# Kernel tuning notes

Hardware: AMD Instinct MI355X
Metric: run time of the kernel (lower is better)

The kernel has to match this reference:

```python
import jax, jax.numpy as jnp
import numpy as np

B, C, O, H, W = 4, 64, 64, 96, 320


def _conv(x, w, b):
    # NCHW conv, stride 1, SAME padding (matches pad=kernel//2 in the torch code)
    out = jax.lax.conv_general_dilated(x, w, (1, 1), 'SAME',
                                       dimension_numbers=('NCHW', 'OIHW', 'NCHW'))
    return out + b[None, :, None, None]


def setup_inputs() -> dict:
    key = jax.random.key(0)
    ks = jax.random.split(key, 18)
    s = 0.05  # small init so learned offsets stay in a realistic few-pixel range
    d = {}
    d['x'] = jax.random.normal(ks[0], (B, C, H, W), jnp.float32)
    d['scale_box2d'] = jax.random.uniform(ks[1], (B, 5), jnp.float32, 0.0, 100.0)
    d['glob_w1'] = jax.random.normal(ks[2], (64, 2), jnp.float32) * s
    d['glob_b1'] = jnp.zeros((64,), jnp.float32)
    d['glob_w2'] = jax.random.normal(ks[3], (32, 64), jnp.float32) * s
    d['glob_b2'] = jnp.zeros((32,), jnp.float32)
    d['loc_w1'] = jax.random.normal(ks[4], (32, C, 3, 3), jnp.float32) * s
    d['loc_b1'] = jnp.zeros((32,), jnp.float32)
    d['loc_w2'] = jax.random.normal(ks[5], (32, 32, 1, 1), jnp.float32) * s
    d['loc_b2'] = jnp.zeros((32,), jnp.float32)
    d['fuse_w1'] = jax.random.normal(ks[6], (32, 64, 3, 3), jnp.float32) * s
    d['fuse_b1'] = jnp.zeros((32,), jnp.float32)
    d['fuse_w2'] = jax.random.normal(ks[7], (18, 32, 1, 1), jnp.float32) * s
    d['fuse_b2'] = jnp.zeros((18,), jnp.float32)
    d['mask_w'] = jnp.full((9, C, 3, 3), 0.5, jnp.float32)  # matches init_mask in torch code
    d['mask_b'] = jnp.zeros((9,), jnp.float32)
    d['conv_w'] = jax.random.normal(ks[8], (O, C, 3, 3), jnp.float32) * s
    d['conv_b'] = jax.random.normal(ks[9], (O,), jnp.float32) * s
    return d


def _deform_conv2d(x, offset, mask, weight, bias):
    # torchvision.ops.deform_conv2d, 3x3 kernel, stride 1, pad 1, dilation 1,
    # one offset group. offset channels are (dy, dx) interleaved per kernel tap.
    b, c, h, w = x.shape
    K = 9
    off = offset.reshape(b, K, 2, h, w)
    dy, dx = off[:, :, 0], off[:, :, 1]            # [B,K,H,W]
    ki = jnp.arange(3, dtype=jnp.float32) - 1.0     # kernel tap offsets with pad=1
    ky = jnp.repeat(ki, 3)                          # [9] row-major taps
    kx = jnp.tile(ki, 3)
    ys = jnp.arange(h, dtype=jnp.float32)[None, None, :, None] + ky[None, :, None, None] + dy
    xs = jnp.arange(w, dtype=jnp.float32)[None, None, None, :] + kx[None, :, None, None] + dx

    y0 = jnp.floor(ys).astype(jnp.int32)
    x0 = jnp.floor(xs).astype(jnp.int32)
    wy = (ys - y0.astype(jnp.float32))[:, None]     # [B,1,K,H,W]
    wx = (xs - x0.astype(jnp.float32))[:, None]

    xf = x.reshape(b, c, h * w)

    def gather(yi, xi):
        valid = ((yi >= 0) & (yi < h) & (xi >= 0) & (xi < w))
        yc = jnp.clip(yi, 0, h - 1)
        xc = jnp.clip(xi, 0, w - 1)
        idx = (yc * w + xc).reshape(b, 1, K * h * w)
        g = jnp.take_along_axis(xf, idx, axis=2).reshape(b, c, K, h, w)
        return g * valid.astype(x.dtype)[:, None]

    val = (gather(y0, x0) * (1 - wy) * (1 - wx)
           + gather(y0, x0 + 1) * (1 - wy) * wx
           + gather(y0 + 1, x0) * wy * (1 - wx)
           + gather(y0 + 1, x0 + 1) * wy * wx)   # [B,C,K,H,W]

    val = val * mask[:, None]                      # modulation mask [B,1,K,H,W]
    out = jnp.einsum('bckhw,ock->bohw', val, weight.reshape(weight.shape[0], c, K))
    return out + bias[None, :, None, None]


def reference(x, scale_box2d, glob_w1, glob_b1, glob_w2, glob_b2,
              loc_w1, loc_b1, loc_w2, loc_b2,
              fuse_w1, fuse_b1, fuse_w2, fuse_b2,
              mask_w, mask_b, conv_w, conv_b):
    b, c, h, w = x.shape
    bsize = jnp.stack([scale_box2d[:, 4] - scale_box2d[:, 2],
                       scale_box2d[:, 3] - scale_box2d[:, 1]], axis=-1)  # [B,2]
    g = jax.nn.relu(bsize @ glob_w1.T + glob_b1) @ glob_w2.T + glob_b2   # [B,32]
    g_offset = jnp.broadcast_to(g[:, :, None, None], (b, 32, h, w))
    l = _conv(jax.nn.relu(_conv(x, loc_w1, loc_b1)), loc_w2, loc_b2)     # [B,32,H,W]
    f = jax.nn.relu(_conv(jnp.concatenate([g_offset, l], axis=1), fuse_w1, fuse_b1))
    offset = _conv(f, fuse_w2, fuse_b2)                                  # [B,18,H,W]
    mask = jax.nn.sigmoid(_conv(x, mask_w, mask_b))                      # [B,9,H,W]
    return _deform_conv2d(x, offset, mask, conv_w, conv_b)
```

## Files before the change

kernel.cpp:

```cpp
#include <hip/hip_runtime.h>
#include <hip/hip_bf16.h>
#include <math.h>

#define BB 4
#define CC 64
#define OO 64
#define HH 96
#define WW 320
#define HWP (HH*WW)
#define NPIX (BB*HWP)

typedef __attribute__((ext_vector_type(8))) short bf16x8;
typedef __attribute__((ext_vector_type(4))) float f32x4;

__device__ inline unsigned short f2bf(float f) {
    unsigned int u = __float_as_uint(f);
    u = (u + 0x7FFFu + ((u >> 16) & 1u)) >> 16;
    return (unsigned short)u;
}
__device__ inline float bf2f(unsigned short s) {
    return __uint_as_float(((unsigned int)s) << 16);
}

__global__ void k_glob(const float* __restrict__ sb,
                       const float* __restrict__ gw1, const float* __restrict__ gb1,
                       const float* __restrict__ gw2, const float* __restrict__ gb2,
                       const float* __restrict__ fw1,
                       float* __restrict__ gsum) {
    __shared__ float g_s[BB * 32];
    int tid = threadIdx.x;
    if (tid < 128) {
        int b = tid >> 5, i = tid & 31;
        float b0 = sb[b * 5 + 4] - sb[b * 5 + 2];
        float b1 = sb[b * 5 + 3] - sb[b * 5 + 1];
        float acc = gb2[i];
        for (int j = 0; j < 64; ++j) {
            float h1 = b0 * gw1[j * 2 + 0] + b1 * gw1[j * 2 + 1] + gb1[j];
            h1 = fmaxf(h1, 0.f);
            acc += gw2[i * 64 + j] * h1;
        }
        g_s[b * 32 + i] = acc;
    }
    __syncthreads();
    for (int e = tid; e < BB * 32 * 9; e += blockDim.x) {
        int b = e / 288, r = e % 288, o = r / 9, k = r % 9;
        float s = 0.f;
        for (int ci = 0; ci < 32; ++ci)
            s += g_s[b * 32 + ci] * fw1[o * 576 + ci * 9 + k];
        gsum[e] = s;
    }
}

#define PREP_N (36864 + 27648 + 1024 + 9216 + 1024)
__global__ void k_prep(const float* __restrict__ cw,
                       const float* __restrict__ lw1, const float* __restrict__ mw,
                       const float* __restrict__ lw2,
                       const float* __restrict__ fw1, const float* __restrict__ fw2,
                       unsigned short* __restrict__ cwT,
                       unsigned short* __restrict__ Wlm,
                       unsigned short* __restrict__ lw2T,
                       unsigned short* __restrict__ Wf,
                       unsigned short* __restrict__ fw2A) {
    int e = blockIdx.x * 256 + threadIdx.x;
    if (e < 36864) {
        int k = e >> 12, r = e & 4095, o = r >> 6, ci = r & 63;
        cwT[e] = f2bf(cw[o * 576 + ci * 9 + k]);
        return;
    }
    e -= 36864;
    if (e < 27648) {
        int k = e / 3072, r = e % 3072, row = r >> 6, ci = r & 63;
        float v = 0.f;
        if (row < 32) v = lw1[row * 576 + ci * 9 + k];
        else if (row < 41) v = mw[(row - 32) * 576 + ci * 9 + k];
        Wlm[e] = f2bf(v);
        return;
    }
    e -= 27648;
    if (e < 1024) { lw2T[e] = f2bf(lw2[e]); return; }
    e -= 1024;
    if (e < 9216) {
        int k = e >> 10, r = e & 1023, o = r >> 5, cl = r & 31;
        Wf[e] = f2bf(fw1[o * 576 + (32 + cl) * 9 + k]);
        return;
    }
    e -= 9216;
    if (e < 1024) {
        int m = e >> 5, ci = e & 31;
        fw2A[e] = f2bf(m < 18 ? fw2[m * 32 + ci] : 0.f);
    }
}

__global__ __launch_bounds__(256) void k_xT(const float* __restrict__ x,
                                            unsigned short* __restrict__ xT) {
    __shared__ unsigned short Ls[64 * 66];
    int tid = threadIdx.x;
    int p0 = blockIdx.x * 64;
    int b = p0 / HWP;
    int rem0 = p0 % HWP;
    int px = tid & 63;
    int g4 = tid >> 6;
    const float* xb = x + (size_t)b * CC * HWP + rem0;
#pragma unroll
    for (int it = 0; it < 16; ++it) {
        int ci = it * 4 + g4;
        Ls[px * 66 + ci] = f2bf(xb[(size_t)ci * HWP + px]);
    }
    __syncthreads();
#pragma unroll
    for (int it = 0; it < 16; ++it) {
        int p = it * 4 + g4;
        xT[(size_t)(p0 + p) * 64 + px] = Ls[p * 66 + px];
    }
}

__global__ __launch_bounds__(256) void k_locmask(
        const unsigned short* __restrict__ xT,
        const unsigned short* __restrict__ Wlm,
        const unsigned short* __restrict__ lw2T,
        const float* __restrict__ lb1, const float* __restrict__ lb2,
        const float* __restrict__ mb,
        unsigned short* __restrict__ lT, unsigned short* __restrict__ mbuf) {
    __shared__ unsigned short Vs[128 * 72];
    __shared__ unsigned short Ws[48 * 72];
    __shared__ unsigned short VsL[128 * 40];
    __shared__ unsigned short W2[32 * 40];

    int tid = threadIdx.x;
    int p0 = blockIdx.x * 128;
    int rem0 = p0 % HWP;

    int lane = tid & 63, wv = tid >> 6;
    int lr = lane & 15, lq = lane >> 4;
    int n0 = wv * 32;

    int spx = tid >> 1;
    int shf = tid & 1;
    int sy = (rem0 + spx) / WW;
    int sx = (rem0 + spx) % WW;

    f32x4 acc[3][2];
#pragma unroll
    for (int mt = 0; mt < 3; ++mt)
#pragma unroll
        for (int t = 0; t < 2; ++t) acc[mt][t] = (f32x4){0.f, 0.f, 0.f, 0.f};

    for (int k = 0; k < 9; ++k) {
        int dy = k / 3 - 1, dx = k % 3 - 1;
        __syncthreads();
#pragma unroll
        for (int c = tid; c < 384; c += 256) {
            int row = c >> 3, g = c & 7;
            *(float4*)&Ws[row * 72 + g * 8] =
                *(const float4*)&Wlm[((size_t)k * 48 + row) * 64 + g * 8];
        }
        {
            int yy = sy + dy, xw = sx + dx;
            bool valid = (yy >= 0) && (yy < HH) && (xw >= 0) && (xw < WW);
            unsigned short* dst = &Vs[spx * 72 + shf * 32];
            if (valid) {
                const unsigned short* src =
                    xT + ((size_t)(p0 + spx) + (dy * WW + dx)) * 64 + shf * 32;
#pragma unroll
                for (int j = 0; j < 4; ++j)
                    *(float4*)(dst + j * 8) = *(const float4*)(src + j * 8);
            } else {
                float4 z = {0.f, 0.f, 0.f, 0.f};
#pragma unroll
                for (int j = 0; j < 4; ++j) *(float4*)(dst + j * 8) = z;
            }
        }
        __syncthreads();
#pragma unroll
        for (int h = 0; h < 2; ++h) {
            bf16x8 b0 = *(const bf16x8*)&Vs[(n0 + lr) * 72 + h * 32 + lq * 8];
            bf16x8 b1 = *(const bf16x8*)&Vs[(n0 + 16 + lr) * 72 + h * 32 + lq * 8];
#pragma unroll
            for (int mt = 0; mt < 3; ++mt) {
                bf16x8 a = *(const bf16x8*)&Ws[(mt * 16 + lr) * 72 + h * 32 + lq * 8];
                acc[mt][0] = __builtin_amdgcn_mfma_f32_16x16x32_bf16(a, b0, acc[mt][0], 0, 0, 0);
                acc[mt][1] = __builtin_amdgcn_mfma_f32_16x16x32_bf16(a, b1, acc[mt][1], 0, 0, 0);
            }
        }
    }

#pragma unroll
    for (int c = tid; c < 128; c += 256) {
        int row = c >> 2, g = c & 3;
        *(float4*)&W2[row * 40 + g * 8] = *(const float4*)&lw2T[row * 32 + g * 8];
    }
#pragma unroll
    for (int mt = 0; mt < 2; ++mt)
#pragma unroll
        for (int t = 0; t < 2; ++t)
#pragma unroll
            for (int r = 0; r < 4; ++r) {
                int m = mt * 16 + lq * 4 + r;
                float v = acc[mt][t][r] + lb1[m];
                VsL[(n0 + t * 16 + lr) * 40 + m] = f2bf(fmaxf(v, 0.f));
            }
#pragma unroll
    for (int t = 0; t < 2; ++t)
#pragma unroll
        for (int r = 0; r < 4; ++r) {
            int j = lq * 4 + r;
            if (j < 9) {
                float v = acc[2][t][r] + mb[j];
                v = 1.f / (1.f + __expf(-v));
                mbuf[(size_t)j * NPIX + p0 + n0 + t * 16 + lr] = f2bf(v);
            }
        }
    __syncthreads();
    f32x4 acc2[2][2];
#pragma unroll
    for (int mt = 0; mt < 2; ++mt)
#pragma unroll
        for (int t = 0; t < 2; ++t) acc2[mt][t] = (f32x4){0.f, 0.f, 0.f, 0.f};
#pragma unroll
    for (int t = 0; t < 2; ++t) {
        bf16x8 b2 = *(const bf16x8*)&VsL[(n0 + t * 16 + lr) * 40 + lq * 8];
#pragma unroll
        for (int mt = 0; mt < 2; ++mt) {
            bf16x8 a2 = *(const bf16x8*)&W2[(mt * 16 + lr) * 40 + lq * 8];
            acc2[mt][t] = __builtin_amdgcn_mfma_f32_16x16x32_bf16(a2, b2, acc2[mt][t], 0, 0, 0);
        }
    }
    __syncthreads();
#pragma unroll
    for (int mt = 0; mt < 2; ++mt)
#pragma unroll
        for (int t = 0; t < 2; ++t)
#pragma unroll
            for (int r = 0; r < 4; ++r) {
                int m = mt * 16 + lq * 4 + r;
                Vs[(n0 + t * 16 + lr) * 40 + m] = f2bf(acc2[mt][t][r] + lb2[m]);
            }
    __syncthreads();
    {
        int px = tid >> 1, hf = tid & 1;
        float4 v0 = *(const float4*)&Vs[px * 40 + hf * 16];
        float4 v1 = *(const float4*)&Vs[px * 40 + hf * 16 + 8];
        unsigned short* dst = lT + (size_t)(p0 + px) * 32 + hf * 16;
        *(float4*)dst = v0;
        *(float4*)(dst + 8) = v1;
    }
}

__global__ __launch_bounds__(256) void k_fuse(
        const unsigned short* __restrict__ lT,
        const float* __restrict__ gsum,
        const unsigned short* __restrict__ Wf,
        const unsigned short* __restrict__ fw2A,
        const float* __restrict__ fb1, const float* __restrict__ fb2,
        float* __restrict__ ysA, float* __restrict__ xsA) {
    __shared__ unsigned short Vs[128 * 40];
    __shared__ unsigned short Ws[32 * 40];
    __shared__ unsigned short VsF[128 * 40];
    __shared__ unsigned short W2[32 * 40];
    __shared__ float gs[288];

    int tid = threadIdx.x;
    int p0 = blockIdx.x * 128;
    int b = p0 / HWP;
    int rem0 = p0 % HWP;

    int lane = tid & 63, wv = tid >> 6;
    int lr = lane & 15, lq = lane >> 4;
    int n0 = wv * 32;

    int spx = tid >> 1;
    int shf = tid & 1;
    int sy = (rem0 + spx) / WW;
    int sx = (rem0 + spx) % WW;

    for (int e = tid; e < 288; e += 256) gs[e] = gsum[b * 288 + e];

    f32x4 acc[2][2];
#pragma unroll
    for (int mt = 0; mt < 2; ++mt)
#pragma unroll
        for (int t = 0; t < 2; ++t) acc[mt][t] = (f32x4){0.f, 0.f, 0.f, 0.f};

    for (int k = 0; k < 9; ++k) {
        int dy = k / 3 - 1, dx = k % 3 - 1;
        __syncthreads();
#pragma unroll
        for (int c = tid; c < 128; c += 256) {
            int row = c >> 2, g = c & 3;
            *(float4*)&Ws[row * 40 + g * 8] =
                *(const float4*)&Wf[((size_t)k * 32 + row) * 32 + g * 8];
        }
        {
            int yy = sy + dy, xw = sx + dx;
            bool valid = (yy >= 0) && (yy < HH) && (xw >= 0) && (xw < WW);
            unsigned short* dst = &Vs[spx * 40 + shf * 16];
            if (valid) {
                const unsigned short* src =
                    lT + ((size_t)(p0 + spx) + (dy * WW + dx)) * 32 + shf * 16;
                *(float4*)dst = *(const float4*)src;
                *(float4*)(dst + 8) = *(const float4*)(src + 8);
            } else {
                float4 z = {0.f, 0.f, 0.f, 0.f};
                *(float4*)dst = z;
                *(float4*)(dst + 8) = z;
            }
        }
        __syncthreads();
#pragma unroll
        for (int t = 0; t < 2; ++t) {
            bf16x8 bfr = *(const bf16x8*)&Vs[(n0 + t * 16 + lr) * 40 + lq * 8];
#pragma unroll
            for (int mt = 0; mt < 2; ++mt) {
                bf16x8 a = *(const bf16x8*)&Ws[(mt * 16 + lr) * 40 + lq * 8];
                acc[mt][t] = __builtin_amdgcn_mfma_f32_16x16x32_bf16(a, bfr, acc[mt][t], 0, 0, 0);
            }
        }
    }

#pragma unroll
    for (int c = tid; c < 128; c += 256) {
        int row = c >> 2, g = c & 3;
        *(float4*)&W2[row * 40 + g * 8] = *(const float4*)&fw2A[row * 32 + g * 8];
    }
#pragma unroll
    for (int t = 0; t < 2; ++t) {
        int px = n0 + t * 16 + lr;
        int rem = rem0 + px;
        int y = rem / WW, xx = rem % WW;
        bool vk[9];
#pragma unroll
        for (int k = 0; k < 9; ++k) {
            int yy = y + k / 3 - 1, xw = xx + k % 3 - 1;
            vk[k] = (yy >= 0) && (yy < HH) && (xw >= 0) && (xw < WW);
        }
#pragma unroll
        for (int mt = 0; mt < 2; ++mt)
#pragma unroll
            for (int r = 0; r < 4; ++r) {
                int m = mt * 16 + lq * 4 + r;
                float s = fb1[m];
#pragma unroll
                for (int k = 0; k < 9; ++k)
                    if (vk[k]) s += gs[m * 9 + k];
                float v = acc[mt][t][r] + s;
                VsF[px * 40 + m] = f2bf(fmaxf(v, 0.f));
            }
    }
    __syncthreads();
    f32x4 acc3[2][2];
#pragma unroll
    for (int mt = 0; mt < 2; ++mt)
#pragma unroll
        for (int t = 0; t < 2; ++t) acc3[mt][t] = (f32x4){0.f, 0.f, 0.f, 0.f};
#pragma unroll
    for (int t = 0; t < 2; ++t) {
        bf16x8 b2 = *(const bf16x8*)&VsF[(n0 + t * 16 + lr) * 40 + lq * 8];
#pragma unroll
        for (int mt = 0; mt < 2; ++mt) {
            bf16x8 a2 = *(const bf16x8*)&W2[(mt * 16 + lr) * 40 + lq * 8];
            acc3[mt][t] = __builtin_amdgcn_mfma_f32_16x16x32_bf16(a2, b2, acc3[mt][t], 0, 0, 0);
        }
    }
#pragma unroll
    for (int t = 0; t < 2; ++t) {
        int px = n0 + t * 16 + lr;
        int p = p0 + px;
        int rem = rem0 + px;
        int y = rem / WW, xx = rem % WW;
#pragma unroll
        for (int mt = 0; mt < 2; ++mt)
#pragma unroll
            for (int r = 0; r < 4; ++r) {
                int m = mt * 16 + lq * 4 + r;
                if (m < 18) {
                    int k = m >> 1;
                    float v = acc3[mt][t][r] + fb2[m];
                    if ((m & 1) == 0)
                        ysA[(size_t)k * NPIX + p] = (float)(y + k / 3 - 1) + v;
                    else
                        xsA[(size_t)k * NPIX + p] = (float)(xx + k % 3 - 1) + v;
                }
            }
    }
}

__global__ __launch_bounds__(256) void k_deform(
        const unsigned short* __restrict__ xT,
        const unsigned short* __restrict__ cwT, const float* __restrict__ cb,
        const float* __restrict__ ysA, const float* __restrict__ xsA,
        const unsigned short* __restrict__ mA, float* __restrict__ out) {
    __shared__ unsigned short Vs[64 * 72];
    __shared__ unsigned short Ws[64 * 72];
    __shared__ float4 cfA[9 * 64];
    __shared__ int4   igA[9 * 64];

    int tid = threadIdx.x;
    int p0 = blockIdx.x * 64;
    int b = p0 / HWP;
    int rem0 = p0 % HWP;
    const unsigned short* xTb = xT + (size_t)b * HWP * 64;

    for (int e = tid; e < 9 * 64; e += 256) {
        int k = e / 64, px = e % 64;
        int p = p0 + px;
        float ys = ysA[(size_t)k * NPIX + p];
        float xs = xsA[(size_t)k * NPIX + p];
        float mk = bf2f(mA[(size_t)k * NPIX + p]);
        float y0f = floorf(ys), x0f = floorf(xs);
        int y0 = (int)y0f, x0 = (int)x0f;
        float wy = ys - y0f, wx = xs - x0f;
        float c00 = (1.f - wy) * (1.f - wx) * mk;
        float c01 = (1.f - wy) * wx * mk;
        float c10 = wy * (1.f - wx) * mk;
        float c11 = wy * wx * mk;
        bool vy0 = (y0 >= 0) && (y0 < HH);
        bool vy1 = (y0 + 1 >= 0) && (y0 + 1 < HH);
        bool vx0 = (x0 >= 0) && (x0 < WW);
        bool vx1 = (x0 + 1 >= 0) && (x0 + 1 < WW);
        c00 = (vy0 && vx0) ? c00 : 0.f;
        c01 = (vy0 && vx1) ? c01 : 0.f;
        c10 = (vy1 && vx0) ? c10 : 0.f;
        c11 = (vy1 && vx1) ? c11 : 0.f;
        int yc0 = min(max(y0, 0), HH - 1), yc1 = min(max(y0 + 1, 0), HH - 1);
        int xc0 = min(max(x0, 0), WW - 1), xc1 = min(max(x0 + 1, 0), WW - 1);
        cfA[e] = make_float4(c00, c01, c10, c11);
        igA[e] = make_int4((yc0 * WW + xc0) * 64, (yc0 * WW + xc1) * 64,
                           (yc1 * WW + xc0) * 64, (yc1 * WW + xc1) * 64);
    }

    int lane = tid & 63;
    int wv = tid >> 6;
    int m0 = wv * 16;
    int lr = lane & 15;
    int lq = lane >> 4;

    f32x4 cini;
    cini[0] = cb[m0 + lq * 4 + 0];
    cini[1] = cb[m0 + lq * 4 + 1];
    cini[2] = cb[m0 + lq * 4 + 2];
    cini[3] = cb[m0 + lq * 4 + 3];
    f32x4 acc[4];
#pragma unroll
    for (int t = 0; t < 4; ++t) acc[t] = cini;

    int sgc = tid & 15;
    int sci0 = sgc * 4;
    int spx = tid >> 4;

    for (int k = 0; k < 9; ++k) {
        __syncthreads();
#pragma unroll
        for (int c = tid; c < 512; c += 256) {
            int o = c >> 3, g = c & 7;
            *(float4*)&Ws[o * 72 + g * 8] = ((const float4*)(cwT + (size_t)k * 4096))[c];
        }
#pragma unroll
        for (int q = 0; q < 4; ++q) {
            int px = q * 16 + spx;
            float4 cc = cfA[k * 64 + px];
            int4 ii = igA[k * 64 + px];
            ushort4 u00 = *(const ushort4*)&xTb[ii.x + sci0];
            ushort4 u01 = *(const ushort4*)&xTb[ii.y + sci0];
            ushort4 u10 = *(const ushort4*)&xTb[ii.z + sci0];
            ushort4 u11 = *(const ushort4*)&xTb[ii.w + sci0];
            ushort4 r;
            r.x = f2bf(cc.x * bf2f(u00.x) + cc.y * bf2f(u01.x) + cc.z * bf2f(u10.x) + cc.w * bf2f(u11.x));
            r.y = f2bf(cc.x * bf2f(u00.y) + cc.y * bf2f(u01.y) + cc.z * bf2f(u10.y) + cc.w * bf2f(u11.y));
            r.z = f2bf(cc.x * bf2f(u00.z) + cc.y * bf2f(u01.z) + cc.z * bf2f(u10.z) + cc.w * bf2f(u11.z));
            r.w = f2bf(cc.x * bf2f(u00.w) + cc.y * bf2f(u01.w) + cc.z * bf2f(u10.w) + cc.w * bf2f(u11.w));
            *(ushort4*)&Vs[px * 72 + sci0] = r;
        }
        __syncthreads();
        bf16x8 a0 = *(const bf16x8*)&Ws[(m0 + lr) * 72 + lq * 8];
        bf16x8 a1 = *(const bf16x8*)&Ws[(m0 + lr) * 72 + 32 + lq * 8];
#pragma unroll
        for (int t = 0; t < 4; ++t) {
            bf16x8 b0 = *(const bf16x8*)&Vs[(t * 16 + lr) * 72 + lq * 8];
            bf16x8 b1 = *(const bf16x8*)&Vs[(t * 16 + lr) * 72 + 32 + lq * 8];
            acc[t] = __builtin_amdgcn_mfma_f32_16x16x32_bf16(a0, b0, acc[t], 0, 0, 0);
            acc[t] = __builtin_amdgcn_mfma_f32_16x16x32_bf16(a1, b1, acc[t], 0, 0, 0);
        }
    }

#pragma unroll
    for (int t = 0; t < 4; ++t) {
#pragma unroll
        for (int r = 0; r < 4; ++r) {
            int o = m0 + lq * 4 + r;
            out[(size_t)(b * 64 + o) * HWP + rem0 + t * 16 + lr] = acc[t][r];
        }
    }
}

extern "C" void kernel_launch(void* const* d_in, const int* in_sizes, int n_in,
                              void* d_out, int out_size, void* d_ws, size_t ws_size,
                              hipStream_t stream) {
    const float* x   = (const float*)d_in[0];
    const float* sb  = (const float*)d_in[1];
    const float* gw1 = (const float*)d_in[2];
    const float* gb1 = (const float*)d_in[3];
    const float* gw2 = (const float*)d_in[4];
    const float* gb2 = (const float*)d_in[5];
    const float* lw1 = (const float*)d_in[6];
    const float* lb1 = (const float*)d_in[7];
    const float* lw2 = (const float*)d_in[8];
    const float* lb2 = (const float*)d_in[9];
    const float* fw1 = (const float*)d_in[10];
    const float* fb1 = (const float*)d_in[11];
    const float* fw2 = (const float*)d_in[12];
    const float* fb2 = (const float*)d_in[13];
    const float* mw  = (const float*)d_in[14];
    const float* mb  = (const float*)d_in[15];
    const float* cw  = (const float*)d_in[16];
    const float* cb  = (const float*)d_in[17];
    float* out = (float*)d_out;

    char* w = (char*)d_ws;
    float* gsum = (float*)w;                 w += 1152 * 4;
    unsigned short* cwT  = (unsigned short*)w; w += 36864 * 2;
    unsigned short* Wlm  = (unsigned short*)w; w += 27648 * 2;
    unsigned short* lw2T = (unsigned short*)w; w += 1024 * 2;
    unsigned short* Wf   = (unsigned short*)w; w += 9216 * 2;
    unsigned short* fw2A = (unsigned short*)w; w += 1024 * 2;
    unsigned short* mbuf = (unsigned short*)w; w += (size_t)9 * NPIX * 2;
    float* ysA = (float*)w;                  w += (size_t)9 * NPIX * 4;
    float* xsA = (float*)w;                  w += (size_t)9 * NPIX * 4;
    unsigned short* xT = (unsigned short*)w; w += (size_t)NPIX * 64 * 2;
    unsigned short* lT = (unsigned short*)w;

    k_prep<<<(PREP_N + 255) / 256, 256, 0, stream>>>(cw, lw1, mw, lw2, fw1, fw2,
                                                     cwT, Wlm, lw2T, Wf, fw2A);
    k_glob<<<1, 128, 0, stream>>>(sb, gw1, gb1, gw2, gb2, fw1, gsum);
    k_xT<<<NPIX / 64, 256, 0, stream>>>(x, xT);
    k_locmask<<<NPIX / 128, 256, 0, stream>>>(xT, Wlm, lw2T, lb1, lb2, mb, lT, mbuf);
    k_fuse<<<NPIX / 128, 256, 0, stream>>>(lT, gsum, Wf, fw2A, fb1, fb2, ysA, xsA);
    k_deform<<<NPIX / 64, 256, 0, stream>>>(xT, cwT, cb, ysA, xsA, mbuf, out);
}
```

Measured before the change: 217.4 us.

## Pack offsets as bf16 pairs, register-resident deform sampling, vectorized transpose, merge glob into prep

The offset output is now stored as packed bf16 (dy,dx) pairs in one uint32 array instead of two fp32 coordinate arrays, and the deform kernel rebuilds absolute coordinates itself. The deform kernel drops its shared-memory staging and barriers: each lane samples its own pixel's 8-channel fragments straight into MFMA B operands and reads weights from global memory. The x transpose uses float4 loads and 16-byte stores, and the tiny glob kernel becomes an extra block of the prep launch, removing one launch. Storing offsets in bf16 loses precision in the sampling positions, and weights are now re-read from global/L2 per wave.

```diff
diff --git a/kernel.cpp b/kernel.cpp
--- a/kernel.cpp
+++ b/kernel.cpp
@@ -11,6 +11,7 @@
 #define NPIX (BB*HWP)
 
 typedef __attribute__((ext_vector_type(8))) short bf16x8;
+typedef __attribute__((ext_vector_type(8))) unsigned short u16x8;
 typedef __attribute__((ext_vector_type(4))) float f32x4;
 
 __device__ inline unsigned short f2bf(float f) {
@@ -22,46 +23,47 @@
     return __uint_as_float(((unsigned int)s) << 16);
 }
 
-__global__ void k_glob(const float* __restrict__ sb,
-                       const float* __restrict__ gw1, const float* __restrict__ gb1,
-                       const float* __restrict__ gw2, const float* __restrict__ gb2,
-                       const float* __restrict__ fw1,
-                       float* __restrict__ gsum) {
-    __shared__ float g_s[BB * 32];
-    int tid = threadIdx.x;
-    if (tid < 128) {
-        int b = tid >> 5, i = tid & 31;
-        float b0 = sb[b * 5 + 4] - sb[b * 5 + 2];
-        float b1 = sb[b * 5 + 3] - sb[b * 5 + 1];
-        float acc = gb2[i];
-        for (int j = 0; j < 64; ++j) {
-            float h1 = b0 * gw1[j * 2 + 0] + b1 * gw1[j * 2 + 1] + gb1[j];
-            h1 = fmaxf(h1, 0.f);
-            acc += gw2[i * 64 + j] * h1;
-        }
-        g_s[b * 32 + i] = acc;
-    }
-    __syncthreads();
-    for (int e = tid; e < BB * 32 * 9; e += blockDim.x) {
-        int b = e / 288, r = e % 288, o = r / 9, k = r % 9;
-        float s = 0.f;
-        for (int ci = 0; ci < 32; ++ci)
-            s += g_s[b * 32 + ci] * fw1[o * 576 + ci * 9 + k];
-        gsum[e] = s;
-    }
-}
-
 #define PREP_N (36864 + 27648 + 1024 + 9216 + 1024)
+#define PREP_BLOCKS ((PREP_N + 255) / 256)
 __global__ void k_prep(const float* __restrict__ cw,
                        const float* __restrict__ lw1, const float* __restrict__ mw,
                        const float* __restrict__ lw2,
                        const float* __restrict__ fw1, const float* __restrict__ fw2,
+                       const float* __restrict__ sb,
+                       const float* __restrict__ gw1, const float* __restrict__ gb1,
+                       const float* __restrict__ gw2, const float* __restrict__ gb2,
                        unsigned short* __restrict__ cwT,
                        unsigned short* __restrict__ Wlm,
                        unsigned short* __restrict__ lw2T,
                        unsigned short* __restrict__ Wf,
-                       unsigned short* __restrict__ fw2A) {
-    int e = blockIdx.x * 256 + threadIdx.x;
+                       unsigned short* __restrict__ fw2A,
+                       float* __restrict__ gsum) {
+    __shared__ float g_s[BB * 32];
+    int tid = threadIdx.x;
+    if (blockIdx.x == PREP_BLOCKS) {
+        if (tid < 128) {
+            int b = tid >> 5, i = tid & 31;
+            float b0 = sb[b * 5 + 4] - sb[b * 5 + 2];
+            float b1 = sb[b * 5 + 3] - sb[b * 5 + 1];
+            float acc = gb2[i];
+            for (int j = 0; j < 64; ++j) {
+                float h1 = b0 * gw1[j * 2 + 0] + b1 * gw1[j * 2 + 1] + gb1[j];
+                h1 = fmaxf(h1, 0.f);
+                acc += gw2[i * 64 + j] * h1;
+            }
+            g_s[b * 32 + i] = acc;
+        }
+        __syncthreads();
+        for (int e = tid; e < BB * 32 * 9; e += 256) {
+            int b = e / 288, r = e % 288, o = r / 9, k = r % 9;
+            float s = 0.f;
+            for (int ci = 0; ci < 32; ++ci)
+                s += g_s[b * 32 + ci] * fw1[o * 576 + ci * 9 + k];
+            gsum[e] = s;
+        }
+        return;
+    }
+    int e = blockIdx.x * 256 + tid;
     if (e < 36864) {
         int k = e >> 12, r = e & 4095, o = r >> 6, ci = r & 63;
         cwT[e] = f2bf(cw[o * 576 + ci * 9 + k]);
@@ -93,24 +95,32 @@
 
 __global__ __launch_bounds__(256) void k_xT(const float* __restrict__ x,
                                             unsigned short* __restrict__ xT) {
-    __shared__ unsigned short Ls[64 * 66];
+    __shared__ unsigned short Ls[64 * 68];
     int tid = threadIdx.x;
     int p0 = blockIdx.x * 64;
     int b = p0 / HWP;
     int rem0 = p0 % HWP;
+    const float* xb = x + (size_t)b * CC * HWP + rem0;
+    int px4 = (tid & 15) * 4;
+    int cib = tid >> 4;
+#pragma unroll
+    for (int it = 0; it < 4; ++it) {
+        int ci = it * 16 + cib;
+        float4 v = *(const float4*)&xb[(size_t)ci * HWP + px4];
+        ushort4 u;
+        u.x = f2bf(v.x); u.y = f2bf(v.y); u.z = f2bf(v.z); u.w = f2bf(v.w);
+        *(ushort4*)&Ls[ci * 68 + px4] = u;
+    }
+    __syncthreads();
     int px = tid & 63;
-    int g4 = tid >> 6;
-    const float* xb = x + (size_t)b * CC * HWP + rem0;
-#pragma unroll
-    for (int it = 0; it < 16; ++it) {
-        int ci = it * 4 + g4;
-        Ls[px * 66 + ci] = f2bf(xb[(size_t)ci * HWP + px]);
-    }
-    __syncthreads();
-#pragma unroll
-    for (int it = 0; it < 16; ++it) {
-        int p = it * 4 + g4;
-        xT[(size_t)(p0 + p) * 64 + px] = Ls[p * 66 + px];
+    int cg = tid >> 6;
+#pragma unroll
+    for (int j = 0; j < 2; ++j) {
+        int ci0 = cg * 16 + j * 8;
+        u16x8 r;
+#pragma unroll
+        for (int i = 0; i < 8; ++i) r[i] = Ls[(ci0 + i) * 68 + px];
+        *(u16x8*)&xT[((size_t)p0 + px) * 64 + ci0] = r;
     }
 }
 
@@ -252,7 +262,7 @@
         const unsigned short* __restrict__ Wf,
         const unsigned short* __restrict__ fw2A,
         const float* __restrict__ fb1, const float* __restrict__ fb2,
-        float* __restrict__ ysA, float* __restrict__ xsA) {
+        unsigned int* __restrict__ dA) {
     __shared__ unsigned short Vs[128 * 40];
     __shared__ unsigned short Ws[32 * 40];
     __shared__ unsigned short VsF[128 * 40];
@@ -363,22 +373,17 @@
     }
 #pragma unroll
     for (int t = 0; t < 2; ++t) {
-        int px = n0 + t * 16 + lr;
-        int p = p0 + px;
-        int rem = rem0 + px;
-        int y = rem / WW, xx = rem % WW;
+        int p = p0 + n0 + t * 16 + lr;
 #pragma unroll
         for (int mt = 0; mt < 2; ++mt)
 #pragma unroll
-            for (int r = 0; r < 4; ++r) {
-                int m = mt * 16 + lq * 4 + r;
+            for (int rr = 0; rr < 4; rr += 2) {
+                int m = mt * 16 + lq * 4 + rr;
                 if (m < 18) {
-                    int k = m >> 1;
-                    float v = acc3[mt][t][r] + fb2[m];
-                    if ((m & 1) == 0)
-                        ysA[(size_t)k * NPIX + p] = (float)(y + k / 3 - 1) + v;
-                    else
-                        xsA[(size_t)k * NPIX + p] = (float)(xx + k % 3 - 1) + v;
+                    float dyv = acc3[mt][t][rr] + fb2[m];
+                    float dxv = acc3[mt][t][rr + 1] + fb2[m + 1];
+                    dA[(size_t)(m >> 1) * NPIX + p] =
+                        (unsigned)f2bf(dyv) | ((unsigned)f2bf(dxv) << 16);
                 }
             }
     }
@@ -387,25 +392,41 @@
 __global__ __launch_bounds__(256) void k_deform(
         const unsigned short* __restrict__ xT,
         const unsigned short* __restrict__ cwT, const float* __restrict__ cb,
-        const float* __restrict__ ysA, const float* __restrict__ xsA,
+        const unsigned int* __restrict__ dA,
         const unsigned short* __restrict__ mA, float* __restrict__ out) {
-    __shared__ unsigned short Vs[64 * 72];
-    __shared__ unsigned short Ws[64 * 72];
-    __shared__ float4 cfA[9 * 64];
-    __shared__ int4   igA[9 * 64];
-
     int tid = threadIdx.x;
     int p0 = blockIdx.x * 64;
     int b = p0 / HWP;
     int rem0 = p0 % HWP;
+    int lane = tid & 63;
+    int wv = tid >> 6;
+    int lr = lane & 15;
+    int lq = lane >> 4;
+    int px = wv * 16 + lr;
+    int p = p0 + px;
+    int rem = rem0 + px;
+    int y = rem / WW, xx = rem % WW;
     const unsigned short* xTb = xT + (size_t)b * HWP * 64;
 
-    for (int e = tid; e < 9 * 64; e += 256) {
-        int k = e / 64, px = e % 64;
-        int p = p0 + px;
-        float ys = ysA[(size_t)k * NPIX + p];
-        float xs = xsA[(size_t)k * NPIX + p];
-        float mk = bf2f(mA[(size_t)k * NPIX + p]);
+    f32x4 acc[4];
+#pragma unroll
+    for (int mt = 0; mt < 4; ++mt) {
+#pragma unroll
+        for (int r = 0; r < 4; ++r) acc[mt][r] = cb[mt * 16 + lq * 4 + r];
+    }
+
+    unsigned int duA[9];
+    float mkA[9];
+#pragma unroll
+    for (int k = 0; k < 9; ++k) {
+        duA[k] = dA[(size_t)k * NPIX + p];
+        mkA[k] = bf2f(mA[(size_t)k * NPIX + p]);
+    }
+
+    for (int k = 0; k < 9; ++k) {
+        float mk = mkA[k];
+        float ys = (float)(y + k / 3 - 1) + bf2f((unsigned short)(duA[k] & 0xffffu));
+        float xs = (float)(xx + k % 3 - 1) + bf2f((unsigned short)(duA[k] >> 16));
         float y0f = floorf(ys), x0f = floorf(xs);
         int y0 = (int)y0f, x0 = (int)x0f;
         float wy = ys - y0f, wx = xs - x0f;
@@ -423,71 +444,38 @@
         c11 = (vy1 && vx1) ? c11 : 0.f;
         int yc0 = min(max(y0, 0), HH - 1), yc1 = min(max(y0 + 1, 0), HH - 1);
         int xc0 = min(max(x0, 0), WW - 1), xc1 = min(max(x0 + 1, 0), WW - 1);
-        cfA[e] = make_float4(c00, c01, c10, c11);
-        igA[e] = make_int4((yc0 * WW + xc0) * 64, (yc0 * WW + xc1) * 64,
-                           (yc1 * WW + xc0) * 64, (yc1 * WW + xc1) * 64);
-    }
-
-    int lane = tid & 63;
-    int wv = tid >> 6;
-    int m0 = wv * 16;
-    int lr = lane & 15;
-    int lq = lane >> 4;
-
-    f32x4 cini;
-    cini[0] = cb[m0 + lq * 4 + 0];
-    cini[1] = cb[m0 + lq * 4 + 1];
-    cini[2] = cb[m0 + lq * 4 + 2];
-    cini[3] = cb[m0 + lq * 4 + 3];
-    f32x4 acc[4];
-#pragma unroll
-    for (int t = 0; t < 4; ++t) acc[t] = cini;
-
-    int sgc = tid & 15;
-    int sci0 = sgc * 4;
-    int spx = tid >> 4;
-
-    for (int k = 0; k < 9; ++k) {
-        __syncthreads();
-#pragma unroll
-        for (int c = tid; c < 512; c += 256) {
-            int o = c >> 3, g = c & 7;
-            *(float4*)&Ws[o * 72 + g * 8] = ((const float4*)(cwT + (size_t)k * 4096))[c];
-        }
-#pragma unroll
-        for (int q = 0; q < 4; ++q) {
-            int px = q * 16 + spx;
-            float4 cc = cfA[k * 64 + px];
-            int4 ii = igA[k * 64 + px];
-            ushort4 u00 = *(const ushort4*)&xTb[ii.x + sci0];
-            ushort4 u01 = *(const ushort4*)&xTb[ii.y + sci0];
-            ushort4 u10 = *(const ushort4*)&xTb[ii.z + sci0];
-            ushort4 u11 = *(const ushort4*)&xTb[ii.w + sci0];
-            ushort4 r;
-            r.x = f2bf(cc.x * bf2f(u00.x) + cc.y * bf2f(u01.x) + cc.z * bf2f(u10.x) + cc.w * bf2f(u11.x));
-            r.y = f2bf(cc.x * bf2f(u00.y) + cc.y * bf2f(u01.y) + cc.z * bf2f(u10.y) + cc.w * bf2f(u11.y));
-            r.z = f2bf(cc.x * bf2f(u00.z) + cc.y * bf2f(u01.z) + cc.z * bf2f(u10.z) + cc.w * bf2f(u11.z));
-            r.w = f2bf(cc.x * bf2f(u00.w) + cc.y * bf2f(u01.w) + cc.z * bf2f(u10.w) + cc.w * bf2f(u11.w));
-            *(ushort4*)&Vs[px * 72 + sci0] = r;
-        }
-        __syncthreads();
-        bf16x8 a0 = *(const bf16x8*)&Ws[(m0 + lr) * 72 + lq * 8];
-        bf16x8 a1 = *(const bf16x8*)&Ws[(m0 + lr) * 72 + 32 + lq * 8];
-#pragma unroll
-        for (int t = 0; t < 4; ++t) {
-            bf16x8 b0 = *(const bf16x8*)&Vs[(t * 16 + lr) * 72 + lq * 8];
-            bf16x8 b1 = *(const bf16x8*)&Vs[(t * 16 + lr) * 72 + 32 + lq * 8];
-            acc[t] = __builtin_amdgcn_mfma_f32_16x16x32_bf16(a0, b0, acc[t], 0, 0, 0);
-            acc[t] = __builtin_amdgcn_mfma_f32_16x16x32_bf16(a1, b1, acc[t], 0, 0, 0);
-        }
-    }
-
-#pragma unroll
-    for (int t = 0; t < 4; ++t) {
+        int i00 = (yc0 * WW + xc0) * 64, i01 = (yc0 * WW + xc1) * 64;
+        int i10 = (yc1 * WW + xc0) * 64, i11 = (yc1 * WW + xc1) * 64;
+
+#pragma unroll
+        for (int h = 0; h < 2; ++h) {
+            int cb_ = h * 32 + lq * 8;
+            u16x8 s00 = *(const u16x8*)(xTb + i00 + cb_);
+            u16x8 s01 = *(const u16x8*)(xTb + i01 + cb_);
+            u16x8 s10 = *(const u16x8*)(xTb + i10 + cb_);
+            u16x8 s11 = *(const u16x8*)(xTb + i11 + cb_);
+            bf16x8 bfrag;
+#pragma unroll
+            for (int j = 0; j < 8; ++j) {
+                float v = c00 * bf2f(s00[j]) + c01 * bf2f(s01[j]) +
+                          c10 * bf2f(s10[j]) + c11 * bf2f(s11[j]);
+                bfrag[j] = (short)f2bf(v);
+            }
+            const unsigned short* wk = cwT + (size_t)k * 4096 + cb_;
+#pragma unroll
+            for (int mt = 0; mt < 4; ++mt) {
+                bf16x8 a = *(const bf16x8*)&wk[(mt * 16 + lr) * 64];
+                acc[mt] = __builtin_amdgcn_mfma_f32_16x16x32_bf16(a, bfrag, acc[mt], 0, 0, 0);
+            }
+        }
+    }
+
+#pragma unroll
+    for (int mt = 0; mt < 4; ++mt) {
 #pragma unroll
         for (int r = 0; r < 4; ++r) {
-            int o = m0 + lq * 4 + r;
-            out[(size_t)(b * 64 + o) * HWP + rem0 + t * 16 + lr] = acc[t][r];
+            int o = mt * 16 + lq * 4 + r;
+            out[(size_t)(b * 64 + o) * HWP + rem] = acc[mt][r];
         }
     }
 }
@@ -516,23 +504,22 @@
     float* out = (float*)d_out;
 
     char* w = (char*)d_ws;
-    float* gsum = (float*)w;                 w += 1152 * 4;
+    float* gsum = (float*)w;                   w += 1152 * 4;
     unsigned short* cwT  = (unsigned short*)w; w += 36864 * 2;
     unsigned short* Wlm  = (unsigned short*)w; w += 27648 * 2;
     unsigned short* lw2T = (unsigned short*)w; w += 1024 * 2;
     unsigned short* Wf   = (unsigned short*)w; w += 9216 * 2;
     unsigned short* fw2A = (unsigned short*)w; w += 1024 * 2;
     unsigned short* mbuf = (unsigned short*)w; w += (size_t)9 * NPIX * 2;
-    float* ysA = (float*)w;                  w += (size_t)9 * NPIX * 4;
-    float* xsA = (float*)w;                  w += (size_t)9 * NPIX * 4;
-    unsigned short* xT = (unsigned short*)w; w += (size_t)NPIX * 64 * 2;
+    unsigned int* dA = (unsigned int*)w;       w += (size_t)9 * NPIX * 4;
+    unsigned short* xT = (unsigned short*)w;   w += (size_t)NPIX * 64 * 2;
     unsigned short* lT = (unsigned short*)w;
 
-    k_prep<<<(PREP_N + 255) / 256, 256, 0, stream>>>(cw, lw1, mw, lw2, fw1, fw2,
-                                                     cwT, Wlm, lw2T, Wf, fw2A);
-    k_glob<<<1, 128, 0, stream>>>(sb, gw1, gb1, gw2, gb2, fw1, gsum);
+    k_prep<<<PREP_BLOCKS + 1, 256, 0, stream>>>(cw, lw1, mw, lw2, fw1, fw2,
+                                                sb, gw1, gb1, gw2, gb2,
+                                                cwT, Wlm, lw2T, Wf, fw2A, gsum);
     k_xT<<<NPIX / 64, 256, 0, stream>>>(x, xT);
     k_locmask<<<NPIX / 128, 256, 0, stream>>>(xT, Wlm, lw2T, lb1, lb2, mb, lT, mbuf);
-    k_fuse<<<NPIX / 128, 256, 0, stream>>>(lT, gsum, Wf, fw2A, fb1, fb2, ysA, xsA);
-    k_deform<<<NPIX / 64, 256, 0, stream>>>(xT, cwT, cb, ysA, xsA, mbuf, out);
-}
+    k_fuse<<<NPIX / 128, 256, 0, stream>>>(lT, gsum, Wf, fw2A, fb1, fb2, dA);
+    k_deform<<<NPIX / 64, 256, 0, stream>>>(xT, cwT, cb, dA, mbuf, out);
+}
```

Result: slower. 293.7 us (+35.1%).
